# Kernel tuning notes

Hardware: AMD Instinct MI355X
Metric: run time of the kernel (lower is better)

The kernel has to match this reference:

```python
import jax, jax.numpy as jnp
import numpy as np

NUM_CAPS = 8
IN_CH = 768
OUT_CH = 64  # == num_routes
BATCH = 16384


def setup_inputs() -> dict:
    key = jax.random.key(0)
    ks = jax.random.split(key, 9)
    lim = 1.0 / np.sqrt(IN_CH)  # torch Linear default init range
    inp = {
        'img_emb': jax.random.normal(ks[0], (BATCH, IN_CH), jnp.float32),
        'capt_emb': jax.random.normal(ks[1], (BATCH, IN_CH), jnp.float32),
        'dct_emb': jax.random.normal(ks[2], (BATCH, IN_CH), jnp.float32),
        'W_img': jax.random.uniform(ks[3], (NUM_CAPS, OUT_CH, IN_CH), jnp.float32, -lim, lim),
        'b_img': jax.random.uniform(ks[4], (NUM_CAPS, OUT_CH), jnp.float32, -lim, lim),
        'W_capt': jax.random.uniform(ks[5], (NUM_CAPS, OUT_CH, IN_CH), jnp.float32, -lim, lim),
        'b_capt': jax.random.uniform(ks[6], (NUM_CAPS, OUT_CH), jnp.float32, -lim, lim),
        'W_dct': jax.random.uniform(ks[7], (NUM_CAPS, OUT_CH, IN_CH), jnp.float32, -lim, lim),
        'b_dct': jax.random.uniform(ks[8], (NUM_CAPS, OUT_CH), jnp.float32, -lim, lim),
    }
    return inp


def _project(x, W, b):
    # x: [B, I]; W: [C, R, I]; b: [C, R] -> [B, R, C]
    # torch: per-capsule Linear y = x @ W_c.T + b_c, viewed [B, R, 1], cat on last dim
    y = jnp.einsum('bi,cri->brc', x, W) + b.T[None]  # [B, R, C]
    return y


def _squash(u, epsilon=1e-07):
    sq = jnp.sum(u * u, axis=-1, keepdims=True)  # [B, 3R, 1]
    safe_norm = jnp.sqrt(sq + epsilon)
    return sq * u / ((1.0 + sq) * safe_norm)


def reference(img_emb, capt_emb, dct_emb, W_img, b_img, W_capt, b_capt, W_dct, b_dct):
    u_img = _project(img_emb, W_img, b_img)      # [B, 64, 8]
    u_capt = _project(capt_emb, W_capt, b_capt)  # [B, 64, 8]
    u_dct = _project(dct_emb, W_dct, b_dct)      # [B, 64, 8]
    combined = jnp.concatenate([u_img, u_capt, u_dct], axis=1)  # [B, 192, 8]
    return _squash(combined)
```

## Files before the change

kernel.cpp:

```cpp
#include <hip/hip_runtime.h>

typedef __attribute__((ext_vector_type(8))) short short8;
typedef __attribute__((ext_vector_type(4))) float floatx4;
typedef __attribute__((ext_vector_type(4))) unsigned int uintx4;

#if __has_builtin(__builtin_amdgcn_cvt_pk_bf16_f32)
typedef __attribute__((ext_vector_type(2))) __bf16 bf16x2;
__device__ __forceinline__ unsigned int pk_bf16(float a, float b) {
  bf16x2 v = __builtin_amdgcn_cvt_pk_bf16_f32(a, b);
  return __builtin_bit_cast(unsigned int, v);
}
#else
__device__ __forceinline__ unsigned int bf16_1(float f) {
  unsigned int u = __builtin_bit_cast(unsigned int, f);
  return (u + 0x7fffu + ((u >> 16) & 1u)) >> 16;
}
__device__ __forceinline__ unsigned int pk_bf16(float a, float b) {
  return bf16_1(a) | (bf16_1(b) << 16);
}
#endif


__global__ __launch_bounds__(256) void prep_w(
    const float* __restrict__ Wi, const float* __restrict__ Wc, const float* __restrict__ Wd,
    const float* __restrict__ bi, const float* __restrict__ bc, const float* __restrict__ bd,
    uintx4* __restrict__ Bprep, float* __restrict__ biasPrep) {
  const int t = blockIdx.x * 256 + threadIdx.x;
  const int l = t & 63;
  const int frag = t >> 6;
  const int nt = frag & 3;
  const int q = frag >> 2;
  const int ks = q % 24;
  const int q2 = q / 24;
  const int h = q2 & 7;
  const int mod = q2 >> 3;
  const int n16 = h * 4 + nt;
  const float* __restrict__ W = (mod == 0) ? Wi : ((mod == 1) ? Wc : Wd);

  const int n = n16 * 16 + (l & 15);
  const int r = n >> 3;
  const int c = n & 7;
  const int i0 = ks * 32 + (l >> 4) * 8;
  const float* src = W + (size_t)(c * 64 + r) * 768 + i0;
  float4 f0 = *(const float4*)(src);
  float4 f1 = *(const float4*)(src + 4);
  uintx4 p;
  p.x = pk_bf16(f0.x, f0.y);
  p.y = pk_bf16(f0.z, f0.w);
  p.z = pk_bf16(f1.x, f1.y);
  p.w = pk_bf16(f1.z, f1.w);
  Bprep[(size_t)frag * 64 + l] = p;

  if (t < 1536) {
    const int m2 = t >> 9;
    const int nn = t & 511;
    const float* bb = (m2 == 0) ? bi : ((m2 == 1) ? bc : bd);
    biasPrep[t] = bb[(nn & 7) * 64 + (nn >> 3)];
  }
}

#define LOADA(aa, kk)                                                        \
  {                                                                          \
    _Pragma("unroll") for (int mt = 0; mt < 2; ++mt)                         \
        aa[mt] = Afr[((kk) * 2 + mt) * 64 +                                  \
                     ((ln ^ (((kk) * 4 + quad) & 15)) + (quad << 4))];       \
  }

#define LOADB(bb, kk)                                                        \
  {                                                                          \
    _Pragma("unroll") for (int n2 = 0; n2 < 8; ++n2)                         \
        bb[n2] = bbase[(size_t)((n2 >> 2) * 96 + (kk) * 4 + (n2 & 3)) * 64]; \
  }

#define COMP(aa, bb)                                                     \
  {                                                                      \
    _Pragma("unroll") for (int mt = 0; mt < 2; ++mt)                     \
    {                                                                    \
      short8 af = __builtin_bit_cast(short8, aa[mt]);                    \
      _Pragma("unroll") for (int n2 = 0; n2 < 8; ++n2)                   \
          acc[mt][n2] = __builtin_amdgcn_mfma_f32_16x16x32_bf16(         \
              af, __builtin_bit_cast(short8, bb[n2]), acc[mt][n2], 0, 0, \
              0);                                                        \
    }                                                                    \
  }

__global__ __launch_bounds__(256, 3) void caps_fused(
    const float* __restrict__ x0, const float* __restrict__ x1, const float* __restrict__ x2,
    const uintx4* __restrict__ Bprep, const float* __restrict__ biasPrep,
    float* __restrict__ out) {
  __shared__ unsigned long long As64[48 * 128];

  const int tid = threadIdx.x;
  const int bx = blockIdx.x;
  const int mod = bx >> 9;
  const int bm = bx & 511;
  const float* __restrict__ X = (mod == 0) ? x0 : ((mod == 1) ? x1 : x2);

  const float* src = X + (size_t)bm * 32 * 768;
#pragma unroll
  for (int i = 0; i < 24; ++i) {
    const int idx = i * 1024 + tid * 4;
    float4 f = *(const float4*)(src + idx);
    const int m = (unsigned)idx / 768u;
    const int k = idx - m * 768;
    const int ks = k >> 5;
    const int kk = k & 31;
    const int qk = kk >> 3;
    const int jh = (kk >> 2) & 1;
    const int mt = m >> 4;
    const int lnn = m & 15;
    const int p = (ks * 4 + qk) & 15;
    const int slot = (lnn ^ p) + (qk << 4);
    unsigned long long w =
        ((unsigned long long)pk_bf16(f.z, f.w) << 32) | pk_bf16(f.x, f.y);
    As64[(((ks * 2 + mt) * 64 + slot) << 1) + jh] = w;
  }
  __syncthreads();

  const int lane = tid & 63;
  const int ln = lane & 15;
  const int quad = lane >> 4;
  const int wv = tid >> 6;

  const uintx4* Afr = (const uintx4*)As64;
  const uintx4* bbase = Bprep + (size_t)((mod * 8 + wv * 2) * 24) * 4 * 64 + lane;

  floatx4 acc[2][8] = {};
  uintx4 a0[2], a1[2], b0[8], b1[8];

  LOADA(a0, 0);
  LOADB(b0, 0);
#pragma unroll 1
  for (int ks2 = 0; ks2 < 12; ++ks2) {
    const int ks = 2 * ks2;
    LOADA(a1, ks + 1);
    LOADB(b1, ks + 1);
    COMP(a0, b0);
    if (ks2 != 11) {
      LOADA(a0, ks + 2);
      LOADB(b0, ks + 2);
    }
    COMP(a1, b1);
  }

  const int col0 = mod * 512 + wv * 128 + ln;
  float bias[8];
#pragma unroll
  for (int n2 = 0; n2 < 8; ++n2) bias[n2] = biasPrep[col0 + n2 * 16];

#pragma unroll
  for (int mt = 0; mt < 2; ++mt) {
    const size_t rbase = (size_t)(bm * 32 + mt * 16 + quad * 4) * 1536;
#pragma unroll
    for (int n2 = 0; n2 < 8; ++n2) {
      float* op = out + rbase + col0 + n2 * 16;
#pragma unroll
      for (int jj = 0; jj < 4; ++jj) {
        float u = acc[mt][n2][jj] + bias[n2];
        float s = u * u;
        s += __shfl_xor(s, 1);
        s += __shfl_xor(s, 2);
        s += __shfl_xor(s, 4);
        float sc = s / ((1.0f + s) * sqrtf(s + 1e-7f));
        op[(size_t)jj * 1536] = u * sc;
      }
    }
  }
}

extern "C" void kernel_launch(void* const* d_in, const int* in_sizes, int n_in,
                              void* d_out, int out_size, void* d_ws, size_t ws_size,
                              hipStream_t stream) {
  const float* ximg = (const float*)d_in[0];
  const float* xcapt = (const float*)d_in[1];
  const float* xdct = (const float*)d_in[2];
  const float* Wi = (const float*)d_in[3];
  const float* bi = (const float*)d_in[4];
  const float* Wc = (const float*)d_in[5];
  const float* bc = (const float*)d_in[6];
  const float* Wd = (const float*)d_in[7];
  const float* bd = (const float*)d_in[8];

  uintx4* Bprep = (uintx4*)d_ws;
  float* biasPrep = (float*)((char*)d_ws + 2304 * 1024);

  hipLaunchKernelGGL(prep_w, dim3(576), dim3(256), 0, stream,
                     Wi, Wc, Wd, bi, bc, bd, Bprep, biasPrep);
  hipLaunchKernelGGL(caps_fused, dim3(1536), dim3(256), 0, stream,
                     ximg, xcapt, xdct, (const uintx4*)Bprep, biasPrep,
                     (float*)d_out);
}
```

Measured before the change: 97.46 us.

## Reorder weight columns so each lane holds all capsules; halve LDS staging

Weight prep now arranges the output columns so that each lane's eight accumulator fragments cover the eight capsules of one route. The squash norm then becomes an in-register sum with no cross-lane shuffles, and each row is written with two float4 stores instead of scattered scalar stores. The A tile is staged into LDS in two halves of K, which halves shared memory and raises the occupancy hint from 3 to 4. The cost is an extra barrier between the halves and the loss of the explicit double-buffered register prefetch in the MFMA loop.

```diff
diff --git a/kernel.cpp b/kernel.cpp
--- a/kernel.cpp
+++ b/kernel.cpp
@@ -28,20 +28,17 @@
   const int t = blockIdx.x * 256 + threadIdx.x;
   const int l = t & 63;
   const int frag = t >> 6;
-  const int nt = frag & 3;
-  const int q = frag >> 2;
+  const int c = frag & 7;
+  const int q = frag >> 3;
   const int ks = q % 24;
   const int q2 = q / 24;
-  const int h = q2 & 7;
-  const int mod = q2 >> 3;
-  const int n16 = h * 4 + nt;
+  const int h = q2 & 3;
+  const int mod = q2 >> 2;
   const float* __restrict__ W = (mod == 0) ? Wi : ((mod == 1) ? Wc : Wd);
 
-  const int n = n16 * 16 + (l & 15);
-  const int r = n >> 3;
-  const int c = n & 7;
+  const int np = c * 64 + h * 16 + (l & 15);
   const int i0 = ks * 32 + (l >> 4) * 8;
-  const float* src = W + (size_t)(c * 64 + r) * 768 + i0;
+  const float* src = W + (size_t)np * 768 + i0;
   float4 f0 = *(const float4*)(src);
   float4 f1 = *(const float4*)(src + 4);
   uintx4 p;
@@ -53,69 +50,23 @@
 
   if (t < 1536) {
     const int m2 = t >> 9;
-    const int nn = t & 511;
     const float* bb = (m2 == 0) ? bi : ((m2 == 1) ? bc : bd);
-    biasPrep[t] = bb[(nn & 7) * 64 + (nn >> 3)];
+    biasPrep[t] = bb[t & 511];
   }
 }
 
-#define LOADA(aa, kk)                                                        \
-  {                                                                          \
-    _Pragma("unroll") for (int mt = 0; mt < 2; ++mt)                         \
-        aa[mt] = Afr[((kk) * 2 + mt) * 64 +                                  \
-                     ((ln ^ (((kk) * 4 + quad) & 15)) + (quad << 4))];       \
-  }
-
-#define LOADB(bb, kk)                                                        \
-  {                                                                          \
-    _Pragma("unroll") for (int n2 = 0; n2 < 8; ++n2)                         \
-        bb[n2] = bbase[(size_t)((n2 >> 2) * 96 + (kk) * 4 + (n2 & 3)) * 64]; \
-  }
-
-#define COMP(aa, bb)                                                     \
-  {                                                                      \
-    _Pragma("unroll") for (int mt = 0; mt < 2; ++mt)                     \
-    {                                                                    \
-      short8 af = __builtin_bit_cast(short8, aa[mt]);                    \
-      _Pragma("unroll") for (int n2 = 0; n2 < 8; ++n2)                   \
-          acc[mt][n2] = __builtin_amdgcn_mfma_f32_16x16x32_bf16(         \
-              af, __builtin_bit_cast(short8, bb[n2]), acc[mt][n2], 0, 0, \
-              0);                                                        \
-    }                                                                    \
-  }
-
-__global__ __launch_bounds__(256, 3) void caps_fused(
+__global__ __launch_bounds__(256, 4) void caps_fused(
     const float* __restrict__ x0, const float* __restrict__ x1, const float* __restrict__ x2,
     const uintx4* __restrict__ Bprep, const float* __restrict__ biasPrep,
     float* __restrict__ out) {
-  __shared__ unsigned long long As64[48 * 128];
+  __shared__ unsigned long long As64[12 * 2 * 64 * 2];
 
   const int tid = threadIdx.x;
   const int bx = blockIdx.x;
   const int mod = bx >> 9;
   const int bm = bx & 511;
   const float* __restrict__ X = (mod == 0) ? x0 : ((mod == 1) ? x1 : x2);
-
   const float* src = X + (size_t)bm * 32 * 768;
-#pragma unroll
-  for (int i = 0; i < 24; ++i) {
-    const int idx = i * 1024 + tid * 4;
-    float4 f = *(const float4*)(src + idx);
-    const int m = (unsigned)idx / 768u;
-    const int k = idx - m * 768;
-    const int ks = k >> 5;
-    const int kk = k & 31;
-    const int qk = kk >> 3;
-    const int jh = (kk >> 2) & 1;
-    const int mt = m >> 4;
-    const int lnn = m & 15;
-    const int p = (ks * 4 + qk) & 15;
-    const int slot = (lnn ^ p) + (qk << 4);
-    unsigned long long w =
-        ((unsigned long long)pk_bf16(f.z, f.w) << 32) | pk_bf16(f.x, f.y);
-    As64[(((ks * 2 + mt) * 64 + slot) << 1) + jh] = w;
-  }
-  __syncthreads();
 
   const int lane = tid & 63;
   const int ln = lane & 15;
@@ -123,47 +74,78 @@
   const int wv = tid >> 6;
 
   const uintx4* Afr = (const uintx4*)As64;
-  const uintx4* bbase = Bprep + (size_t)((mod * 8 + wv * 2) * 24) * 4 * 64 + lane;
+  const uintx4* bbase = Bprep + (size_t)(mod * 4 + wv) * (24 * 8 * 64) + lane;
 
   floatx4 acc[2][8] = {};
-  uintx4 a0[2], a1[2], b0[8], b1[8];
 
-  LOADA(a0, 0);
-  LOADB(b0, 0);
 #pragma unroll 1
-  for (int ks2 = 0; ks2 < 12; ++ks2) {
-    const int ks = 2 * ks2;
-    LOADA(a1, ks + 1);
-    LOADB(b1, ks + 1);
-    COMP(a0, b0);
-    if (ks2 != 11) {
-      LOADA(a0, ks + 2);
-      LOADB(b0, ks + 2);
+  for (int ph = 0; ph < 2; ++ph) {
+    if (ph) __syncthreads();
+#pragma unroll
+    for (int i = 0; i < 12; ++i) {
+      const int f4 = i * 256 + tid;
+      const int m = f4 / 96;
+      const int k = (f4 - m * 96) * 4;
+      float4 f = *(const float4*)(src + (size_t)m * 768 + ph * 384 + k);
+      const int ks2 = k >> 5;
+      const int kk = k & 31;
+      const int qk = kk >> 3;
+      const int jh = (kk >> 2) & 1;
+      const int mt = m >> 4;
+      const int lnn = m & 15;
+      const int p = (ks2 * 4 + qk) & 15;
+      const int slot = (lnn ^ p) + (qk << 4);
+      unsigned long long w =
+          ((unsigned long long)pk_bf16(f.z, f.w) << 32) | pk_bf16(f.x, f.y);
+      As64[(((ks2 * 2 + mt) * 64 + slot) << 1) + jh] = w;
     }
-    COMP(a1, b1);
+    __syncthreads();
+
+#pragma unroll 1
+    for (int ks2 = 0; ks2 < 12; ++ks2) {
+      const int ks = ph * 12 + ks2;
+      uintx4 b[8], a[2];
+#pragma unroll
+      for (int c = 0; c < 8; ++c) b[c] = bbase[(size_t)(ks * 8 + c) * 64];
+#pragma unroll
+      for (int mt = 0; mt < 2; ++mt)
+        a[mt] = Afr[(ks2 * 2 + mt) * 64 +
+                    ((ln ^ ((ks2 * 4 + quad) & 15)) + (quad << 4))];
+#pragma unroll
+      for (int mt = 0; mt < 2; ++mt) {
+        short8 af = __builtin_bit_cast(short8, a[mt]);
+#pragma unroll
+        for (int c = 0; c < 8; ++c)
+          acc[mt][c] = __builtin_amdgcn_mfma_f32_16x16x32_bf16(
+              af, __builtin_bit_cast(short8, b[c]), acc[mt][c], 0, 0, 0);
+      }
+    }
   }
 
-  const int col0 = mod * 512 + wv * 128 + ln;
+  const float* bp = biasPrep + mod * 512 + wv * 16 + ln;
   float bias[8];
 #pragma unroll
-  for (int n2 = 0; n2 < 8; ++n2) bias[n2] = biasPrep[col0 + n2 * 16];
+  for (int c = 0; c < 8; ++c) bias[c] = bp[c * 64];
 
 #pragma unroll
   for (int mt = 0; mt < 2; ++mt) {
-    const size_t rbase = (size_t)(bm * 32 + mt * 16 + quad * 4) * 1536;
 #pragma unroll
-    for (int n2 = 0; n2 < 8; ++n2) {
-      float* op = out + rbase + col0 + n2 * 16;
+    for (int jj = 0; jj < 4; ++jj) {
+      const size_t row = (size_t)(bm * 32 + mt * 16 + quad * 4 + jj);
+      float u[8];
+      float s = 0.f;
 #pragma unroll
-      for (int jj = 0; jj < 4; ++jj) {
-        float u = acc[mt][n2][jj] + bias[n2];
-        float s = u * u;
-        s += __shfl_xor(s, 1);
-        s += __shfl_xor(s, 2);
-        s += __shfl_xor(s, 4);
-        float sc = s / ((1.0f + s) * sqrtf(s + 1e-7f));
-        op[(size_t)jj * 1536] = u * sc;
+      for (int c = 0; c < 8; ++c) {
+        u[c] = acc[mt][c][jj] + bias[c];
+        s += u[c] * u[c];
       }
+      const float sc = s / ((1.0f + s) * sqrtf(s + 1e-7f));
+      float4 o0, o1;
+      o0.x = u[0] * sc; o0.y = u[1] * sc; o0.z = u[2] * sc; o0.w = u[3] * sc;
+      o1.x = u[4] * sc; o1.y = u[5] * sc; o1.z = u[6] * sc; o1.w = u[7] * sc;
+      float* op = out + row * 1536 + mod * 512 + (size_t)(wv * 16 + ln) * 8;
+      *(float4*)op = o0;
+      *((float4*)(op + 4)) = o1;
     }
   }
 }
```

Measured after the change: 142.7 us. 46.4% more time.

## Reorder weight fragments so each lane holds all 8 capsules; stage output through LDS

Applied to the files above, without the earlier changes.

Rearranges the prepared bf16 weight fragments so that each MFMA column tile corresponds to one capsule index c. The squash reduction over 8 capsules then happens within a single lane's registers instead of through cross-lane shuffles. The epilogue writes results to LDS and then streams full contiguous rows to global memory with nontemporal stores, replacing strided scalar stores. It also adds a block-index swizzle and nontemporal loads for the inputs, at the cost of extra LDS barriers in the epilogue.

```diff
diff --git a/kernel.cpp b/kernel.cpp
--- a/kernel.cpp
+++ b/kernel.cpp
@@ -28,22 +28,19 @@
   const int t = blockIdx.x * 256 + threadIdx.x;
   const int l = t & 63;
   const int frag = t >> 6;
-  const int nt = frag & 3;
-  const int q = frag >> 2;
+  const int c = frag & 7;
+  const int q = frag >> 3;
   const int ks = q % 24;
   const int q2 = q / 24;
-  const int h = q2 & 7;
-  const int mod = q2 >> 3;
-  const int n16 = h * 4 + nt;
+  const int h = q2 & 3;
+  const int mod = q2 >> 2;
   const float* __restrict__ W = (mod == 0) ? Wi : ((mod == 1) ? Wc : Wd);
 
-  const int n = n16 * 16 + (l & 15);
-  const int r = n >> 3;
-  const int c = n & 7;
+  const int np = c * 64 + h * 16 + (l & 15);
   const int i0 = ks * 32 + (l >> 4) * 8;
-  const float* src = W + (size_t)(c * 64 + r) * 768 + i0;
-  float4 f0 = *(const float4*)(src);
-  float4 f1 = *(const float4*)(src + 4);
+  const float* src = W + (size_t)np * 768 + i0;
+  floatx4 f0 = *(const floatx4*)(src);
+  floatx4 f1 = *(const floatx4*)(src + 4);
   uintx4 p;
   p.x = pk_bf16(f0.x, f0.y);
   p.y = pk_bf16(f0.z, f0.w);
@@ -53,9 +50,8 @@
 
   if (t < 1536) {
     const int m2 = t >> 9;
-    const int nn = t & 511;
     const float* bb = (m2 == 0) ? bi : ((m2 == 1) ? bc : bd);
-    biasPrep[t] = bb[(nn & 7) * 64 + (nn >> 3)];
+    biasPrep[t] = bb[t & 511];
   }
 }
 
@@ -68,8 +64,8 @@
 
 #define LOADB(bb, kk)                                                        \
   {                                                                          \
-    _Pragma("unroll") for (int n2 = 0; n2 < 8; ++n2)                         \
-        bb[n2] = bbase[(size_t)((n2 >> 2) * 96 + (kk) * 4 + (n2 & 3)) * 64]; \
+    _Pragma("unroll") for (int c2 = 0; c2 < 8; ++c2)                         \
+        bb[c2] = bbase[(size_t)((kk) * 8 + c2) * 64];                        \
   }
 
 #define COMP(aa, bb)                                                     \
@@ -77,9 +73,9 @@
     _Pragma("unroll") for (int mt = 0; mt < 2; ++mt)                     \
     {                                                                    \
       short8 af = __builtin_bit_cast(short8, aa[mt]);                    \
-      _Pragma("unroll") for (int n2 = 0; n2 < 8; ++n2)                   \
-          acc[mt][n2] = __builtin_amdgcn_mfma_f32_16x16x32_bf16(         \
-              af, __builtin_bit_cast(short8, bb[n2]), acc[mt][n2], 0, 0, \
+      _Pragma("unroll") for (int c2 = 0; c2 < 8; ++c2)                   \
+          acc[mt][c2] = __builtin_amdgcn_mfma_f32_16x16x32_bf16(         \
+              af, __builtin_bit_cast(short8, bb[c2]), acc[mt][c2], 0, 0, \
               0);                                                        \
     }                                                                    \
   }
@@ -91,7 +87,8 @@
   __shared__ unsigned long long As64[48 * 128];
 
   const int tid = threadIdx.x;
-  const int bx = blockIdx.x;
+  const int bx0 = blockIdx.x;
+  const int bx = (bx0 & 7) * 192 + (bx0 >> 3);
   const int mod = bx >> 9;
   const int bm = bx & 511;
   const float* __restrict__ X = (mod == 0) ? x0 : ((mod == 1) ? x1 : x2);
@@ -100,7 +97,7 @@
 #pragma unroll
   for (int i = 0; i < 24; ++i) {
     const int idx = i * 1024 + tid * 4;
-    float4 f = *(const float4*)(src + idx);
+    floatx4 f = __builtin_nontemporal_load((const floatx4*)(src + idx));
     const int m = (unsigned)idx / 768u;
     const int k = idx - m * 768;
     const int ks = k >> 5;
@@ -123,7 +120,7 @@
   const int wv = tid >> 6;
 
   const uintx4* Afr = (const uintx4*)As64;
-  const uintx4* bbase = Bprep + (size_t)((mod * 8 + wv * 2) * 24) * 4 * 64 + lane;
+  const uintx4* bbase = Bprep + (size_t)(mod * 4 + wv) * (24 * 8 * 64) + lane;
 
   floatx4 acc[2][8] = {};
   uintx4 a0[2], a1[2], b0[8], b1[8];
@@ -143,28 +140,44 @@
     COMP(a1, b1);
   }
 
-  const int col0 = mod * 512 + wv * 128 + ln;
+  const float* bp = biasPrep + mod * 512 + wv * 16 + ln;
   float bias[8];
 #pragma unroll
-  for (int n2 = 0; n2 < 8; ++n2) bias[n2] = biasPrep[col0 + n2 * 16];
-
-#pragma unroll
+  for (int c = 0; c < 8; ++c) bias[c] = bp[c * 64];
+
+  float* ldsf = (float*)As64;
+  __syncthreads();
+
+#pragma unroll 1
   for (int mt = 0; mt < 2; ++mt) {
-    const size_t rbase = (size_t)(bm * 32 + mt * 16 + quad * 4) * 1536;
-#pragma unroll
-    for (int n2 = 0; n2 < 8; ++n2) {
-      float* op = out + rbase + col0 + n2 * 16;
-#pragma unroll
-      for (int jj = 0; jj < 4; ++jj) {
-        float u = acc[mt][n2][jj] + bias[n2];
-        float s = u * u;
-        s += __shfl_xor(s, 1);
-        s += __shfl_xor(s, 2);
-        s += __shfl_xor(s, 4);
-        float sc = s / ((1.0f + s) * sqrtf(s + 1e-7f));
-        op[(size_t)jj * 1536] = u * sc;
+#pragma unroll
+    for (int jj = 0; jj < 4; ++jj) {
+      float u[8];
+      float s = 0.f;
+#pragma unroll
+      for (int c = 0; c < 8; ++c) {
+        u[c] = acc[mt][c][jj] + bias[c];
+        s += u[c] * u[c];
       }
+      const float sc = s / ((1.0f + s) * sqrtf(s + 1e-7f));
+      floatx4 o0, o1;
+      o0.x = u[0] * sc; o0.y = u[1] * sc; o0.z = u[2] * sc; o0.w = u[3] * sc;
+      o1.x = u[4] * sc; o1.y = u[5] * sc; o1.z = u[6] * sc; o1.w = u[7] * sc;
+      float* p = ldsf + (quad * 4 + jj) * 512 + (wv * 16 + ln) * 8;
+      *(floatx4*)p = o0;
+      *((floatx4*)(p + 4)) = o1;
     }
+    __syncthreads();
+#pragma unroll
+    for (int i = 0; i < 8; ++i) {
+      const int idx = i * 256 + tid;
+      const int row = idx >> 7;
+      const int cf = (idx & 127) << 2;
+      const floatx4 v = *(const floatx4*)(ldsf + row * 512 + cf);
+      float* gp = out + (size_t)(bm * 32 + mt * 16 + row) * 1536 + mod * 512 + cf;
+      __builtin_nontemporal_store(v, (floatx4*)gp);
+    }
+    if (mt == 0) __syncthreads();
   }
 }
 
```

Measured after the change: 134.8 us. +38.3%, slower.
